# Kernel optimization log

Measured on AMD Instinct MI355X. Metric: run time of the kernel, lower is better.

Reference implementation:

```python
import jax, jax.numpy as jnp
import numpy as np
import math

N = 50000      # nodes
E = 600000     # edges
IN = 128       # in_channels
OUT = 128      # out_channels (heads * per-head)
H = 2          # heads
D = OUT // H   # per-head dim = 64
TDIM = 64      # time encoder out_channels
MSG = 64       # msg_dim
EDGE = TDIM + MSG  # edge_dim = 128


def setup_inputs() -> dict:
    key = jax.random.key(0)
    ks = jax.random.split(key, 16)
    s_in = 1.0 / math.sqrt(IN)
    s_ed = 1.0 / math.sqrt(EDGE)
    return {
        "x": jax.random.normal(ks[0], (N, IN), dtype=jnp.float32),
        "last_update": jax.random.randint(ks[1], (N,), 0, 1000000, dtype=jnp.int32),
        "edge_index": jax.random.randint(ks[2], (2, E), 0, N, dtype=jnp.int64),
        "t": jax.random.randint(ks[3], (E,), 0, 1000000, dtype=jnp.int32),
        "msg": jax.random.normal(ks[4], (E, MSG), dtype=jnp.float32),
        # TimeEncoder: cos(Linear(1 -> TDIM))
        "time_w": jax.random.normal(ks[5], (TDIM,), dtype=jnp.float32) * 0.01,
        "time_b": jax.random.normal(ks[6], (TDIM,), dtype=jnp.float32),
        # TransformerConv params (heads=2, per-head D, edge_dim=EDGE)
        "Wq": jax.random.normal(ks[7], (IN, H * D), dtype=jnp.float32) * s_in,
        "bq": jnp.zeros((H * D,), dtype=jnp.float32),
        "Wk": jax.random.normal(ks[8], (IN, H * D), dtype=jnp.float32) * s_in,
        "bk": jnp.zeros((H * D,), dtype=jnp.float32),
        "Wv": jax.random.normal(ks[9], (IN, H * D), dtype=jnp.float32) * s_in,
        "bv": jnp.zeros((H * D,), dtype=jnp.float32),
        "We": jax.random.normal(ks[10], (EDGE, H * D), dtype=jnp.float32) * s_ed,  # lin_edge, no bias
        "Wskip": jax.random.normal(ks[11], (IN, H * D), dtype=jnp.float32) * s_in,
        "bskip": jnp.zeros((H * D,), dtype=jnp.float32),
    }


def reference(x, last_update, edge_index, t, msg,
              time_w, time_b, Wq, bq, Wk, bk, Wv, bv, We, Wskip, bskip):
    src = edge_index[0]
    dst = edge_index[1]

    # rel_t = last_update[src] - t ; time encoding cos(w * rel_t + b)
    rel_t = (last_update[src] - t).astype(x.dtype)                 # [E]
    rel_t_enc = jnp.cos(rel_t[:, None] * time_w + time_b)          # [E, TDIM]
    edge_attr = jnp.concatenate([rel_t_enc, msg], axis=-1)         # [E, EDGE]

    n = x.shape[0]
    # Node projections, then per-edge gather (PyG: i = dst, j = src)
    q = (x @ Wq + bq).reshape(n, H, D)[dst]                        # [E, H, D]
    k = (x @ Wk + bk).reshape(n, H, D)[src]                        # [E, H, D]
    v = (x @ Wv + bv).reshape(n, H, D)[src]                        # [E, H, D]
    e = (edge_attr @ We).reshape(-1, H, D)                         # [E, H, D]

    k = k + e
    alpha = jnp.sum(q * k, axis=-1) / math.sqrt(D)                 # [E, H]

    # segment softmax over edges sharing the same destination node
    amax = jax.ops.segment_max(alpha, dst, num_segments=n)         # [N, H]
    ex = jnp.exp(alpha - amax[dst])                                # [E, H]
    denom = jax.ops.segment_sum(ex, dst, num_segments=n)           # [N, H]
    attn = ex / (denom[dst] + 1e-16)                               # [E, H]

    out_e = (v + e) * attn[..., None]                              # [E, H, D]
    out = jax.ops.segment_sum(out_e, dst, num_segments=n)          # [N, H, D]
    out = out.reshape(n, H * D)

    # root/skip connection (root_weight=True, beta=False)
    return out + (x @ Wskip + bskip)
```

## Files before the change

### kernel.cpp

```cpp
#include <hip/hip_runtime.h>
#include <hip/hip_bf16.h>

typedef __hip_bfloat16 bf16;
typedef __attribute__((ext_vector_type(8))) short bfrag;
typedef __attribute__((ext_vector_type(4))) float ffrag;

#define CDIM 128
#define TDIMC 64
#define MSGD 64
#define INV2PI 0.15915494309189535f

__device__ __forceinline__ unsigned short f2bf(float f) {
    union { __hip_bfloat16 h; unsigned short u; } cv;
    cv.h = __float2bfloat16(f);
    return cv.u;
}

__device__ __forceinline__ float fcos_rev(float xr) {
    float fr, c;
    asm("v_fract_f32 %0, %1" : "=v"(fr) : "v"(xr));
    asm("v_cos_f32 %0, %1" : "=v"(c) : "v"(fr));
    return c;
}

__global__ void detect_kernel(const int* __restrict__ ei, int samp, int* __restrict__ flag) {
    int i = blockIdx.x * blockDim.x + threadIdx.x;
    if (i < samp) {
        if (ei[2 * i + 1] != 0) atomicOr(flag, 1);
    }
}

__global__ void hist_kernel(const int* __restrict__ ei, int E, const int* __restrict__ flag,
                            int* __restrict__ count) {
    int e = blockIdx.x * 256 + threadIdx.x;
    if (e >= E) return;
    int is32 = *flag;
    int d = is32 ? ei[E + e] : ei[2 * (E + e)];
    atomicAdd(&count[d], 1);
}

__global__ __launch_bounds__(1024)
void scan1_kernel(const int* __restrict__ count, int N,
                  int* __restrict__ cur, int* __restrict__ bsum) {
    __shared__ int wsum[16];
    __shared__ int woff[16];
    int t = threadIdx.x;
    int lane = t & 63, wv = t >> 6;
    int i = blockIdx.x * 1024 + t;
    int v = (i < N) ? count[i] : 0;
    int incl = v;
#pragma unroll
    for (int off = 1; off < 64; off <<= 1) {
        int n = __shfl_up(incl, off, 64);
        if (lane >= off) incl += n;
    }
    if (lane == 63) wsum[wv] = incl;
    __syncthreads();
    if (wv == 0) {
        int ws = (lane < 16) ? wsum[lane] : 0;
        int wi = ws;
#pragma unroll
        for (int off = 1; off < 16; off <<= 1) {
            int n = __shfl_up(wi, off, 64);
            if (lane >= off) wi += n;
        }
        if (lane < 16) woff[lane] = wi - ws;
        if (lane == 15) bsum[blockIdx.x] = wi;
    }
    __syncthreads();
    if (i < N) cur[i] = woff[wv] + incl - v;
}

__global__ void scan2_kernel(int* __restrict__ bsum, int nb) {
    int lane = threadIdx.x;
    int carry = 0;
    for (int base = 0; base < nb; base += 64) {
        int i = base + lane;
        int v = (i < nb) ? bsum[i] : 0;
        int incl = v;
#pragma unroll
        for (int off = 1; off < 64; off <<= 1) {
            int n = __shfl_up(incl, off, 64);
            if (lane >= off) incl += n;
        }
        if (i < nb) bsum[i] = carry + incl - v;
        carry += __shfl(incl, 63, 64);
    }
}

__global__ void scatter_kernel(const int* __restrict__ ei, int E, const int* __restrict__ flag,
                               const int* __restrict__ tarr, const int* __restrict__ last_update,
                               int* __restrict__ cur, const int* __restrict__ bsum,
                               int4* __restrict__ ed_s) {
    int e = blockIdx.x * 256 + threadIdx.x;
    if (e >= E) return;
    int is32 = *flag;
    int s = is32 ? ei[e] : ei[2 * e];
    int d = is32 ? ei[E + e] : ei[2 * (E + e)];
    int pos = atomicAdd(&cur[d], 1) + bsum[d >> 10];
    float rt = (float)(last_update[s] - tarr[e]);
    ed_s[pos] = make_int4(s, d, e, __float_as_int(rt));
}

__global__ void wconv_kernel(const float* __restrict__ Wq, const float* __restrict__ Wk,
                             const float* __restrict__ Wv, const float* __restrict__ Ws,
                             const float* __restrict__ We,
                             short* __restrict__ Wt, short* __restrict__ Wet) {
    int idx = blockIdx.x * 256 + threadIdx.x;
    if (idx >= 5 * 16384) return;
    int mat = idx >> 14;
    int r = idx & 16383;
    int n = r >> 7, kk = r & 127;
    const float* W = (mat == 0) ? Wq : (mat == 1) ? Wk : (mat == 2) ? Wv : (mat == 3) ? Ws : We;
    short bv = (short)f2bf(W[kk * 128 + n]);
    if (mat < 4) Wt[(size_t)mat * 16384 + n * 128 + kk] = bv;
    else         Wet[n * 128 + kk] = bv;
}

__global__ __launch_bounds__(256)
void proj_kernel(const float* __restrict__ x, const short* __restrict__ Wt,
                 const float* __restrict__ bq, const float* __restrict__ bk,
                 const float* __restrict__ bv, const float* __restrict__ bs,
                 float* __restrict__ q, short* __restrict__ kbf, short* __restrict__ vbf,
                 float* __restrict__ out, int N) {
    __shared__ __attribute__((aligned(16))) short sx[64][136];
    int tid = threadIdx.x;
    int n0 = blockIdx.x * 64;
    const float4* x4 = (const float4*)x;
    for (int i = tid; i < 64 * 32; i += 256) {
        int nl = i >> 5, c4 = i & 31;
        int n = n0 + nl;
        float4 f = (n < N) ? x4[(size_t)n * 32 + c4] : make_float4(0.f, 0.f, 0.f, 0.f);
        unsigned int lo = ((unsigned int)f2bf(f.y) << 16) | f2bf(f.x);
        unsigned int hi = ((unsigned int)f2bf(f.w) << 16) | f2bf(f.z);
        *(uint2*)&sx[nl][c4 * 4] = make_uint2(lo, hi);
    }
    __syncthreads();

    int lane = tid & 63, wv = tid >> 6;
    int n15 = lane & 15, quad = lane >> 4;
    const short* W = Wt + (size_t)wv * 16384;
    const float* bias = (wv == 0) ? bq : (wv == 1) ? bk : (wv == 2) ? bv : bs;

    ffrag acc[4][8];
#pragma unroll
    for (int r = 0; r < 4; ++r)
#pragma unroll
        for (int c = 0; c < 8; ++c)
            acc[r][c] = (ffrag){0.f, 0.f, 0.f, 0.f};

#pragma unroll
    for (int kc = 0; kc < 4; ++kc) {
        int kk = kc * 32 + quad * 8;
        bfrag a[4];
#pragma unroll
        for (int r = 0; r < 4; ++r)
            a[r] = *(const bfrag*)&sx[r * 16 + n15][kk];
#pragma unroll
        for (int c = 0; c < 8; ++c) {
            bfrag b = *(const bfrag*)&W[(c * 16 + n15) * 128 + kk];
#pragma unroll
            for (int r = 0; r < 4; ++r)
                acc[r][c] = __builtin_amdgcn_mfma_f32_16x16x32_bf16(a[r], b, acc[r][c], 0, 0, 0);
        }
    }

    if (wv == 1 || wv == 2) {
        short* dsts = (wv == 1) ? kbf : vbf;
#pragma unroll
        for (int c = 0; c < 8; ++c) {
            int col = c * 16 + n15;
            float bval = bias[col];
#pragma unroll
            for (int r = 0; r < 4; ++r) {
#pragma unroll
                for (int g = 0; g < 4; ++g) {
                    int n = n0 + r * 16 + quad * 4 + g;
                    if (n < N) dsts[(size_t)n * CDIM + col] = (short)f2bf(acc[r][c][g] + bval);
                }
            }
        }
    } else {
        float* dstp = (wv == 0) ? q : out;
#pragma unroll
        for (int c = 0; c < 8; ++c) {
            int col = c * 16 + n15;
            float bval = bias[col];
#pragma unroll
            for (int r = 0; r < 4; ++r) {
#pragma unroll
                for (int g = 0; g < 4; ++g) {
                    int n = n0 + r * 16 + quad * 4 + g;
                    if (n < N) dstp[(size_t)n * CDIM + col] = acc[r][c][g] + bval;
                }
            }
        }
    }
}

#define LOADQ(KA, QA, VA, JB) do {                                              \
    _Pragma("unroll")                                                           \
    for (int u = 0; u < 4; ++u) {                                               \
        int el = wv * 16 + (JB) * 4 + u;                                        \
        int s = s_src[el], d = s_dst[el];                                       \
        KA[u] = *(const unsigned int*)&k[(size_t)s * CDIM + 2 * lane];          \
        QA[u] = *(const float2*)&q[(size_t)d * CDIM + 2 * lane];                \
        VA[u] = *(const unsigned int*)&v[(size_t)s * CDIM + 2 * lane];          \
    } } while (0)

#define PROC(KA, QA, VA, JB) do {                                               \
    _Pragma("unroll")                                                           \
    for (int u = 0; u < 4; ++u) {                                               \
        int el = wv * 16 + (JB) * 4 + u;                                        \
        unsigned int ep = *(const unsigned int*)&sbuf[el][2 * lane];            \
        float ex0 = __uint_as_float(ep << 16);                                  \
        float ex1 = __uint_as_float(ep & 0xffff0000u);                          \
        float kx = __uint_as_float(KA[u] << 16) + ex0;                          \
        float ky = __uint_as_float(KA[u] & 0xffff0000u) + ex1;                  \
        float p = QA[u].x * kx + QA[u].y * ky;                                  \
        _Pragma("unroll")                                                       \
        for (int off = 1; off < 32; off <<= 1) p += __shfl_xor(p, off, 32);     \
        float exv = (e0 + el < E) ? __expf(p * 0.125f) : 0.f;                   \
        int d = s_dst[el];                                                      \
        if (d != cur_d) {                              \
            float* np = &num[(size_t)cur_d * CDIM + 2 * lane];                  \
            unsafeAtomicAdd(np, accx);                                          \
            unsafeAtomicAdd(np + 1, accy);                                      \
            if ((lane & 31) == 0) unsafeAtomicAdd(&den[cur_d * 2 + h], dacc);   \
            accx = 0.f; accy = 0.f; dacc = 0.f;                                 \
            cur_d = d;                                                          \
        }                                                                       \
        float vx = __uint_as_float(VA[u] << 16) + ex0;                          \
        float vy = __uint_as_float(VA[u] & 0xffff0000u) + ex1;                  \
        accx = fmaf(vx, exv, accx);                                             \
        accy = fmaf(vy, exv, accy);                                             \
        dacc += exv;                                                            \
    } } while (0)

__global__ __launch_bounds__(256)
void edge_kernel(const int4* __restrict__ ed_s,
                 const float* __restrict__ msg,
                 const float* __restrict__ time_w, const float* __restrict__ time_b,
                 const short* __restrict__ Wet,
                 const float* __restrict__ q, const short* __restrict__ k, const short* __restrict__ v,
                 float* __restrict__ num, float* __restrict__ den,
                 int E) {
    __shared__ __attribute__((aligned(16))) short sbuf[64][136];
    __shared__ int s_src[64], s_dst[64];
    int tid = threadIdx.x;

    int nwg = gridDim.x;
    int q8 = nwg >> 3, r8 = nwg & 7;
    int xcd = blockIdx.x & 7, idx8 = blockIdx.x >> 3;
    int bid = (xcd < r8 ? xcd * (q8 + 1) : r8 * (q8 + 1) + (xcd - r8) * q8) + idx8;
    int e0 = bid * 64;

    if (tid < 64) {
        int4 ed = ed_s[e0 + tid];
        s_src[tid] = ed.x;
        s_dst[tid] = ed.y;
    }
    {
#pragma unroll
        for (int ii = 0; ii < 8; ++ii) {
            int i = tid + ii * 256;
            int el = i >> 5, c2 = i & 31;
            float rt = __int_as_float(ed_s[e0 + el].w);
            float2 w = ((const float2*)time_w)[c2];
            float2 b = ((const float2*)time_b)[c2];
            float c0 = fcos_rev(fmaf(rt, w.x * INV2PI, b.x * INV2PI));
            float c1 = fcos_rev(fmaf(rt, w.y * INV2PI, b.y * INV2PI));
            unsigned int pk = ((unsigned int)f2bf(c1) << 16) | f2bf(c0);
            *(unsigned int*)&sbuf[el][c2 * 2] = pk;
        }
        const float4* msg4 = (const float4*)msg;
#pragma unroll
        for (int jj = 0; jj < 4; ++jj) {
            int j = tid + jj * 256;
            int el = j >> 4, f4 = j & 15;
            int p = ed_s[e0 + el].z;
            float4 m = msg4[(size_t)p * 16 + f4];
            unsigned int lo = ((unsigned int)f2bf(m.y) << 16) | f2bf(m.x);
            unsigned int hi = ((unsigned int)f2bf(m.w) << 16) | f2bf(m.z);
            *(uint2*)&sbuf[el][TDIMC + f4 * 4] = make_uint2(lo, hi);
        }
    }
    __syncthreads();

    int lane = tid & 63;
    int wv = tid >> 6;
    int n15 = lane & 15, quad = lane >> 4;

    unsigned int k0[4], v0[4], k1[4], v1[4], k2[4], v2[4], k3[4], v3[4];
    float2 q0[4], q1[4], q2[4], q3[4];
    LOADQ(k0, q0, v0, 0);
    LOADQ(k1, q1, v1, 1);

    ffrag acc[8];
#pragma unroll
    for (int c = 0; c < 8; ++c) acc[c] = (ffrag){0.f, 0.f, 0.f, 0.f};
#pragma unroll
    for (int kc = 0; kc < 4; ++kc) {
        int kk = kc * 32 + quad * 8;
        bfrag a = *(const bfrag*)&sbuf[wv * 16 + n15][kk];
#pragma unroll
        for (int c = 0; c < 8; ++c) {
            bfrag b = *(const bfrag*)&Wet[(c * 16 + n15) * 128 + kk];
            acc[c] = __builtin_amdgcn_mfma_f32_16x16x32_bf16(a, b, acc[c], 0, 0, 0);
        }
    }
#pragma unroll
    for (int c = 0; c < 8; ++c)
#pragma unroll
        for (int r = 0; r < 4; ++r)
            sbuf[wv * 16 + quad * 4 + r][c * 16 + n15] = (short)f2bf(acc[c][r]);

    asm volatile("s_waitcnt lgkmcnt(0)" ::: "memory");
    __builtin_amdgcn_s_barrier();
    __builtin_amdgcn_sched_barrier(0);

    int h = lane >> 5;
    float accx = 0.f, accy = 0.f, dacc = 0.f;
    int cur_d = s_dst[wv * 16];

    LOADQ(k2, q2, v2, 2);
    PROC(k0, q0, v0, 0);
    LOADQ(k3, q3, v3, 3);
    PROC(k1, q1, v1, 1);
    PROC(k2, q2, v2, 2);
    PROC(k3, q3, v3, 3);

    {
        float* np = &num[(size_t)cur_d * CDIM + 2 * lane];
        unsafeAtomicAdd(np, accx);
        unsafeAtomicAdd(np + 1, accy);
        if ((lane & 31) == 0) unsafeAtomicAdd(&den[cur_d * 2 + h], dacc);
    }
}

__global__ __launch_bounds__(256)
void norm_kernel(const float* __restrict__ num, const float* __restrict__ den,
                 float* __restrict__ out, int N) {
    int idx = blockIdx.x * 256 + threadIdx.x;
    if (idx >= N * 32) return;
    int n = idx >> 5, c4 = idx & 31;
    int h = c4 >> 4;
    float inv = 1.f / (den[n * 2 + h] + 1e-16f);
    float4 nm = ((const float4*)num)[idx];
    float4* op = (float4*)out + idx;
    float4 o = *op;
    o.x = fmaf(nm.x, inv, o.x);
    o.y = fmaf(nm.y, inv, o.y);
    o.z = fmaf(nm.z, inv, o.z);
    o.w = fmaf(nm.w, inv, o.w);
    *op = o;
}

extern "C" void kernel_launch(void* const* d_in, const int* in_sizes, int n_in,
                              void* d_out, int out_size, void* d_ws, size_t ws_size,
                              hipStream_t stream) {
    const float* x       = (const float*)d_in[0];
    const int*   last_up = (const int*)d_in[1];
    const int*   ei      = (const int*)d_in[2];
    const int*   tarr    = (const int*)d_in[3];
    const float* msg     = (const float*)d_in[4];
    const float* time_w  = (const float*)d_in[5];
    const float* time_b  = (const float*)d_in[6];
    const float* Wq = (const float*)d_in[7];  const float* bq = (const float*)d_in[8];
    const float* Wk = (const float*)d_in[9];  const float* bk = (const float*)d_in[10];
    const float* Wv = (const float*)d_in[11]; const float* bv = (const float*)d_in[12];
    const float* We = (const float*)d_in[13];
    const float* Wskip = (const float*)d_in[14]; const float* bskip = (const float*)d_in[15];
    float* out = (float*)d_out;

    int N = in_sizes[0] / CDIM;
    int E = in_sizes[3];
    int nb = (N + 1023) >> 10;

    char* ws = (char*)d_ws;
    size_t off = 0;
#define ALLOC(ptr, type, nelem) type* ptr = (type*)(ws + off); off = (off + (size_t)(nelem) * sizeof(type) + 255) & ~(size_t)255
    ALLOC(q_,    float, (size_t)N * CDIM);
    ALLOC(kbf_,  short, (size_t)N * CDIM);
    ALLOC(vbf_,  short, (size_t)N * CDIM);
    ALLOC(num,   float, (size_t)N * CDIM + 2 * N);
    float* den_ = num + (size_t)N * CDIM;
    ALLOC(count, int,   N + 64);
    int* flag = count + N;
    ALLOC(cur,    int,  N);
    ALLOC(bsum,   int,  nb + 64);
    ALLOC(ed_s,   int4, (size_t)E + 64);
    ALLOC(Wt,     short, 4 * 16384);
    ALLOC(Wet,    short, 16384);
#undef ALLOC

    hipMemsetAsync(count, 0, (size_t)(N + 64) * 4, stream);
    hipMemsetAsync(num, 0, ((size_t)N * CDIM + 2 * N) * sizeof(float), stream);
    hipMemsetAsync(ed_s + E, 0, 64 * sizeof(int4), stream);

    int samp = E < 65536 ? E : 65536;
    detect_kernel<<<(samp + 255) / 256, 256, 0, stream>>>(ei, samp, flag);
    hist_kernel<<<(E + 255) / 256, 256, 0, stream>>>(ei, E, flag, count);
    scan1_kernel<<<nb, 1024, 0, stream>>>(count, N, cur, bsum);
    scan2_kernel<<<1, 64, 0, stream>>>(bsum, nb);
    scatter_kernel<<<(E + 255) / 256, 256, 0, stream>>>(ei, E, flag, tarr, last_up,
                                                        cur, bsum, ed_s);
    wconv_kernel<<<(5 * 16384 + 255) / 256, 256, 0, stream>>>(Wq, Wk, Wv, Wskip, We, Wt, Wet);
    proj_kernel<<<(N + 63) / 64, 256, 0, stream>>>(x, Wt, bq, bk, bv, bskip,
                                                   q_, kbf_, vbf_, out, N);
    edge_kernel<<<(E + 63) / 64, 256, 0, stream>>>(ed_s, msg, time_w, time_b, Wet,
                                                   q_, kbf_, vbf_, num, den_, E);
    norm_kernel<<<(N * 32 + 255) / 256, 256, 0, stream>>>(num, den_, out, N);
}
```

Before: 624.5 us.

## Make edge kernel wave-local, drop block barriers and prefetch gathers early

Each wave now loads its own 16 edges' metadata into LDS and builds its own edge-attribute rows, so the block-wide __syncthreads and s_barrier become per-wave LDS waitcnt fences. The k/q/v gathers and msg loads are issued before the cosine encoding to hide gather latency, and the MFMA section is wrapped in s_setprio. This removes cross-wave stalls at the cost of more live registers. It relies on every wave touching only its own sbuf rows.

```diff
diff --git a/kernel.cpp b/kernel.cpp
--- a/kernel.cpp
+++ b/kernel.cpp
@@ -19,8 +19,13 @@
 __device__ __forceinline__ float fcos_rev(float xr) {
     float fr, c;
     asm("v_fract_f32 %0, %1" : "=v"(fr) : "v"(xr));
-    asm("v_cos_f32 %0, %1" : "=v"(c) : "v"(fr));
+    asm("v_cos_f32 %0, %1" : "=v"(c) : "v"(xr < 0.f ? fr : fr));
     return c;
+}
+
+__device__ __forceinline__ void wave_lds_fence() {
+    asm volatile("s_waitcnt lgkmcnt(0)" ::: "memory");
+    __builtin_amdgcn_sched_barrier(0);
 }
 
 __global__ void detect_kernel(const int* __restrict__ ei, int samp, int* __restrict__ flag) {
@@ -246,8 +251,11 @@
                  float* __restrict__ num, float* __restrict__ den,
                  int E) {
     __shared__ __attribute__((aligned(16))) short sbuf[64][136];
-    __shared__ int s_src[64], s_dst[64];
+    __shared__ int s_src[64], s_dst[64], s_perm[64];
+    __shared__ float s_relt[64];
     int tid = threadIdx.x;
+    int lane = tid & 63;
+    int wv = tid >> 6;
 
     int nwg = gridDim.x;
     int q8 = nwg >> 3, r8 = nwg & 7;
@@ -255,17 +263,36 @@
     int bid = (xcd < r8 ? xcd * (q8 + 1) : r8 * (q8 + 1) + (xcd - r8) * q8) + idx8;
     int e0 = bid * 64;
 
-    if (tid < 64) {
-        int4 ed = ed_s[e0 + tid];
-        s_src[tid] = ed.x;
-        s_dst[tid] = ed.y;
-    }
+    if (lane < 16) {
+        int4 ed = ed_s[e0 + wv * 16 + lane];
+        s_src[wv * 16 + lane] = ed.x;
+        s_dst[wv * 16 + lane] = ed.y;
+        s_perm[wv * 16 + lane] = ed.z;
+        s_relt[wv * 16 + lane] = __int_as_float(ed.w);
+    }
+    wave_lds_fence();
+
+    unsigned int k0[4], v0[4], k1[4], v1[4], k2[4], v2[4], k3[4], v3[4];
+    float2 q0[4], q1[4], q2[4], q3[4];
+    LOADQ(k0, q0, v0, 0);
+    LOADQ(k1, q1, v1, 1);
+
     {
+        const float4* msg4 = (const float4*)msg;
+        float4 m[4];
+        int jel[4], jf4[4];
+#pragma unroll
+        for (int jj = 0; jj < 4; ++jj) {
+            int j = jj * 64 + lane;
+            jel[jj] = wv * 16 + (j >> 4);
+            jf4[jj] = j & 15;
+            m[jj] = msg4[(size_t)s_perm[jel[jj]] * 16 + jf4[jj]];
+        }
 #pragma unroll
         for (int ii = 0; ii < 8; ++ii) {
-            int i = tid + ii * 256;
-            int el = i >> 5, c2 = i & 31;
-            float rt = __int_as_float(ed_s[e0 + el].w);
+            int i = ii * 64 + lane;
+            int el = wv * 16 + (i >> 5), c2 = i & 31;
+            float rt = s_relt[el];
             float2 w = ((const float2*)time_w)[c2];
             float2 b = ((const float2*)time_b)[c2];
             float c0 = fcos_rev(fmaf(rt, w.x * INV2PI, b.x * INV2PI));
@@ -273,32 +300,21 @@
             unsigned int pk = ((unsigned int)f2bf(c1) << 16) | f2bf(c0);
             *(unsigned int*)&sbuf[el][c2 * 2] = pk;
         }
-        const float4* msg4 = (const float4*)msg;
 #pragma unroll
         for (int jj = 0; jj < 4; ++jj) {
-            int j = tid + jj * 256;
-            int el = j >> 4, f4 = j & 15;
-            int p = ed_s[e0 + el].z;
-            float4 m = msg4[(size_t)p * 16 + f4];
-            unsigned int lo = ((unsigned int)f2bf(m.y) << 16) | f2bf(m.x);
-            unsigned int hi = ((unsigned int)f2bf(m.w) << 16) | f2bf(m.z);
-            *(uint2*)&sbuf[el][TDIMC + f4 * 4] = make_uint2(lo, hi);
-        }
-    }
-    __syncthreads();
-
-    int lane = tid & 63;
-    int wv = tid >> 6;
+            unsigned int lo = ((unsigned int)f2bf(m[jj].y) << 16) | f2bf(m[jj].x);
+            unsigned int hi = ((unsigned int)f2bf(m[jj].w) << 16) | f2bf(m[jj].z);
+            *(uint2*)&sbuf[jel[jj]][TDIMC + jf4[jj] * 4] = make_uint2(lo, hi);
+        }
+    }
+    wave_lds_fence();
+
     int n15 = lane & 15, quad = lane >> 4;
 
-    unsigned int k0[4], v0[4], k1[4], v1[4], k2[4], v2[4], k3[4], v3[4];
-    float2 q0[4], q1[4], q2[4], q3[4];
-    LOADQ(k0, q0, v0, 0);
-    LOADQ(k1, q1, v1, 1);
-
     ffrag acc[8];
 #pragma unroll
     for (int c = 0; c < 8; ++c) acc[c] = (ffrag){0.f, 0.f, 0.f, 0.f};
+    __builtin_amdgcn_s_setprio(1);
 #pragma unroll
     for (int kc = 0; kc < 4; ++kc) {
         int kk = kc * 32 + quad * 8;
@@ -309,15 +325,14 @@
             acc[c] = __builtin_amdgcn_mfma_f32_16x16x32_bf16(a, b, acc[c], 0, 0, 0);
         }
     }
+    __builtin_amdgcn_s_setprio(0);
 #pragma unroll
     for (int c = 0; c < 8; ++c)
 #pragma unroll
         for (int r = 0; r < 4; ++r)
             sbuf[wv * 16 + quad * 4 + r][c * 16 + n15] = (short)f2bf(acc[c][r]);
 
-    asm volatile("s_waitcnt lgkmcnt(0)" ::: "memory");
-    __builtin_amdgcn_s_barrier();
-    __builtin_amdgcn_sched_barrier(0);
+    wave_lds_fence();
 
     int h = lane >> 5;
     float accx = 0.f, accy = 0.f, dacc = 0.f;
```

Result: slower. 671.9 us (+7.6%).

## Fuse prep kernels, merge scatter into projection, interleave K/V rows

Applied to the files above, without the earlier changes.

Folds the int64/int32 detection, histogram and weight conversion into one prep kernel, and puts the edge scatter into the projection kernel as extra blocks. K and V are stored interleaved per node so the edge kernel fetches both with a single 8-byte gather instead of two 4-byte gathers. Padding memsets are dropped by clamping edge indices, and the count buffer is zeroed with the same memset as num/den. This cuts launch count and gather transactions. Detecting the index width per wavefront with a ballot is less robust than the old global sample.

```diff
diff --git a/kernel.cpp b/kernel.cpp
--- a/kernel.cpp
+++ b/kernel.cpp
@@ -9,6 +9,7 @@
 #define TDIMC 64
 #define MSGD 64
 #define INV2PI 0.15915494309189535f
+#define WCONV_BLOCKS 320
 
 __device__ __forceinline__ unsigned short f2bf(float f) {
     union { __hip_bfloat16 h; unsigned short u; } cv;
@@ -23,20 +24,32 @@
     return c;
 }
 
-__global__ void detect_kernel(const int* __restrict__ ei, int samp, int* __restrict__ flag) {
-    int i = blockIdx.x * blockDim.x + threadIdx.x;
-    if (i < samp) {
-        if (ei[2 * i + 1] != 0) atomicOr(flag, 1);
-    }
-}
-
-__global__ void hist_kernel(const int* __restrict__ ei, int E, const int* __restrict__ flag,
-                            int* __restrict__ count) {
-    int e = blockIdx.x * 256 + threadIdx.x;
-    if (e >= E) return;
-    int is32 = *flag;
-    int d = is32 ? ei[E + e] : ei[2 * (E + e)];
-    atomicAdd(&count[d], 1);
+__global__ __launch_bounds__(256)
+void prep_kernel(const int* __restrict__ ei, int E, int* __restrict__ count,
+                 const float* __restrict__ Wq, const float* __restrict__ Wk,
+                 const float* __restrict__ Wv, const float* __restrict__ Ws,
+                 const float* __restrict__ We,
+                 short* __restrict__ Wt, short* __restrict__ Wet) {
+    int b = blockIdx.x;
+    if (b < WCONV_BLOCKS) {
+        int idx = b * 256 + threadIdx.x;
+        if (idx >= 5 * 16384) return;
+        int mat = idx >> 14;
+        int r = idx & 16383;
+        int n = r >> 7, kk = r & 127;
+        const float* W = (mat == 0) ? Wq : (mat == 1) ? Wk : (mat == 2) ? Wv : (mat == 3) ? Ws : We;
+        short bv = (short)f2bf(W[kk * 128 + n]);
+        if (mat < 4) Wt[(size_t)mat * 16384 + n * 128 + kk] = bv;
+        else         Wet[n * 128 + kk] = bv;
+    } else {
+        int e = (b - WCONV_BLOCKS) * 256 + threadIdx.x;
+        int probe = (e < E) ? ei[2 * e + 1] : 0;
+        int is32 = (__ballot(probe != 0) != 0ULL);
+        if (e < E) {
+            int d = is32 ? ei[E + e] : ei[2 * (E + e)];
+            atomicAdd(&count[d], 1);
+        }
+    }
 }
 
 __global__ __launch_bounds__(1024)
@@ -88,43 +101,30 @@
     }
 }
 
-__global__ void scatter_kernel(const int* __restrict__ ei, int E, const int* __restrict__ flag,
-                               const int* __restrict__ tarr, const int* __restrict__ last_update,
-                               int* __restrict__ cur, const int* __restrict__ bsum,
-                               int4* __restrict__ ed_s) {
-    int e = blockIdx.x * 256 + threadIdx.x;
-    if (e >= E) return;
-    int is32 = *flag;
-    int s = is32 ? ei[e] : ei[2 * e];
-    int d = is32 ? ei[E + e] : ei[2 * (E + e)];
-    int pos = atomicAdd(&cur[d], 1) + bsum[d >> 10];
-    float rt = (float)(last_update[s] - tarr[e]);
-    ed_s[pos] = make_int4(s, d, e, __float_as_int(rt));
-}
-
-__global__ void wconv_kernel(const float* __restrict__ Wq, const float* __restrict__ Wk,
-                             const float* __restrict__ Wv, const float* __restrict__ Ws,
-                             const float* __restrict__ We,
-                             short* __restrict__ Wt, short* __restrict__ Wet) {
-    int idx = blockIdx.x * 256 + threadIdx.x;
-    if (idx >= 5 * 16384) return;
-    int mat = idx >> 14;
-    int r = idx & 16383;
-    int n = r >> 7, kk = r & 127;
-    const float* W = (mat == 0) ? Wq : (mat == 1) ? Wk : (mat == 2) ? Wv : (mat == 3) ? Ws : We;
-    short bv = (short)f2bf(W[kk * 128 + n]);
-    if (mat < 4) Wt[(size_t)mat * 16384 + n * 128 + kk] = bv;
-    else         Wet[n * 128 + kk] = bv;
-}
-
 __global__ __launch_bounds__(256)
-void proj_kernel(const float* __restrict__ x, const short* __restrict__ Wt,
-                 const float* __restrict__ bq, const float* __restrict__ bk,
-                 const float* __restrict__ bv, const float* __restrict__ bs,
-                 float* __restrict__ q, short* __restrict__ kbf, short* __restrict__ vbf,
-                 float* __restrict__ out, int N) {
+void sp_kernel(const float* __restrict__ x, const short* __restrict__ Wt,
+               const float* __restrict__ bq, const float* __restrict__ bk,
+               const float* __restrict__ bv, const float* __restrict__ bs,
+               float* __restrict__ q, short* __restrict__ kvs,
+               float* __restrict__ out, int N, int PB,
+               const int* __restrict__ ei, int E,
+               const int* __restrict__ tarr, const int* __restrict__ last_update,
+               int* __restrict__ cur, const int* __restrict__ bsum,
+               int4* __restrict__ ed_s) {
     __shared__ __attribute__((aligned(16))) short sx[64][136];
     int tid = threadIdx.x;
+    if (blockIdx.x >= PB) {
+        int e = (blockIdx.x - PB) * 256 + tid;
+        int probe = (e < E) ? ei[2 * e + 1] : 0;
+        int is32 = (__ballot(probe != 0) != 0ULL);
+        if (e >= E) return;
+        int s = is32 ? ei[e] : ei[2 * e];
+        int d = is32 ? ei[E + e] : ei[2 * (E + e)];
+        int pos = atomicAdd(&cur[d], 1) + bsum[d >> 10];
+        float rt = (float)(last_update[s] - tarr[e]);
+        ed_s[pos] = make_int4(s, d, e, __float_as_int(rt));
+        return;
+    }
     int n0 = blockIdx.x * 64;
     const float4* x4 = (const float4*)x;
     for (int i = tid; i < 64 * 32; i += 256) {
@@ -166,17 +166,18 @@
     }
 
     if (wv == 1 || wv == 2) {
-        short* dsts = (wv == 1) ? kbf : vbf;
+        int isv = (wv == 2) ? 2 : 0;
 #pragma unroll
         for (int c = 0; c < 8; ++c) {
             int col = c * 16 + n15;
             float bval = bias[col];
+            int coff = (col >> 1) * 4 + (col & 1) + isv;
 #pragma unroll
             for (int r = 0; r < 4; ++r) {
 #pragma unroll
                 for (int g = 0; g < 4; ++g) {
                     int n = n0 + r * 16 + quad * 4 + g;
-                    if (n < N) dsts[(size_t)n * CDIM + col] = (short)f2bf(acc[r][c][g] + bval);
+                    if (n < N) kvs[(size_t)n * 256 + coff] = (short)f2bf(acc[r][c][g] + bval);
                 }
             }
         }
@@ -198,25 +199,24 @@
     }
 }
 
-#define LOADQ(KA, QA, VA, JB) do {                                              \
+#define LOADQ(KVA, QA, JB) do {                                                 \
     _Pragma("unroll")                                                           \
     for (int u = 0; u < 4; ++u) {                                               \
         int el = wv * 16 + (JB) * 4 + u;                                        \
         int s = s_src[el], d = s_dst[el];                                       \
-        KA[u] = *(const unsigned int*)&k[(size_t)s * CDIM + 2 * lane];          \
+        KVA[u] = kv[(size_t)s * 64 + lane];                                     \
         QA[u] = *(const float2*)&q[(size_t)d * CDIM + 2 * lane];                \
-        VA[u] = *(const unsigned int*)&v[(size_t)s * CDIM + 2 * lane];          \
     } } while (0)
 
-#define PROC(KA, QA, VA, JB) do {                                               \
+#define PROC(KVA, QA, JB) do {                                                  \
     _Pragma("unroll")                                                           \
     for (int u = 0; u < 4; ++u) {                                               \
         int el = wv * 16 + (JB) * 4 + u;                                        \
         unsigned int ep = *(const unsigned int*)&sbuf[el][2 * lane];            \
         float ex0 = __uint_as_float(ep << 16);                                  \
         float ex1 = __uint_as_float(ep & 0xffff0000u);                          \
-        float kx = __uint_as_float(KA[u] << 16) + ex0;                          \
-        float ky = __uint_as_float(KA[u] & 0xffff0000u) + ex1;                  \
+        float kx = __uint_as_float(KVA[u].x << 16) + ex0;                       \
+        float ky = __uint_as_float(KVA[u].x & 0xffff0000u) + ex1;               \
         float p = QA[u].x * kx + QA[u].y * ky;                                  \
         _Pragma("unroll")                                                       \
         for (int off = 1; off < 32; off <<= 1) p += __shfl_xor(p, off, 32);     \
@@ -230,8 +230,8 @@
             accx = 0.f; accy = 0.f; dacc = 0.f;                                 \
             cur_d = d;                                                          \
         }                                                                       \
-        float vx = __uint_as_float(VA[u] << 16) + ex0;                          \
-        float vy = __uint_as_float(VA[u] & 0xffff0000u) + ex1;                  \
+        float vx = __uint_as_float(KVA[u].y << 16) + ex0;                       \
+        float vy = __uint_as_float(KVA[u].y & 0xffff0000u) + ex1;               \
         accx = fmaf(vx, exv, accx);                                             \
         accy = fmaf(vy, exv, accy);                                             \
         dacc += exv;                                                            \
@@ -242,12 +242,13 @@
                  const float* __restrict__ msg,
                  const float* __restrict__ time_w, const float* __restrict__ time_b,
                  const short* __restrict__ Wet,
-                 const float* __restrict__ q, const short* __restrict__ k, const short* __restrict__ v,
+                 const float* __restrict__ q, const uint2* __restrict__ kv,
                  float* __restrict__ num, float* __restrict__ den,
                  int E) {
     __shared__ __attribute__((aligned(16))) short sbuf[64][136];
     __shared__ int s_src[64], s_dst[64];
     int tid = threadIdx.x;
+    int Em1 = E - 1;
 
     int nwg = gridDim.x;
     int q8 = nwg >> 3, r8 = nwg & 7;
@@ -256,7 +257,7 @@
     int e0 = bid * 64;
 
     if (tid < 64) {
-        int4 ed = ed_s[e0 + tid];
+        int4 ed = ed_s[min(e0 + tid, Em1)];
         s_src[tid] = ed.x;
         s_dst[tid] = ed.y;
     }
@@ -265,7 +266,7 @@
         for (int ii = 0; ii < 8; ++ii) {
             int i = tid + ii * 256;
             int el = i >> 5, c2 = i & 31;
-            float rt = __int_as_float(ed_s[e0 + el].w);
+            float rt = __int_as_float(ed_s[min(e0 + el, Em1)].w);
             float2 w = ((const float2*)time_w)[c2];
             float2 b = ((const float2*)time_b)[c2];
             float c0 = fcos_rev(fmaf(rt, w.x * INV2PI, b.x * INV2PI));
@@ -278,7 +279,7 @@
         for (int jj = 0; jj < 4; ++jj) {
             int j = tid + jj * 256;
             int el = j >> 4, f4 = j & 15;
-            int p = ed_s[e0 + el].z;
+            int p = ed_s[min(e0 + el, Em1)].z;
             float4 m = msg4[(size_t)p * 16 + f4];
             unsigned int lo = ((unsigned int)f2bf(m.y) << 16) | f2bf(m.x);
             unsigned int hi = ((unsigned int)f2bf(m.w) << 16) | f2bf(m.z);
@@ -291,10 +292,10 @@
     int wv = tid >> 6;
     int n15 = lane & 15, quad = lane >> 4;
 
-    unsigned int k0[4], v0[4], k1[4], v1[4], k2[4], v2[4], k3[4], v3[4];
+    uint2 kv0[4], kv1[4], kv2[4], kv3[4];
     float2 q0[4], q1[4], q2[4], q3[4];
-    LOADQ(k0, q0, v0, 0);
-    LOADQ(k1, q1, v1, 1);
+    LOADQ(kv0, q0, 0);
+    LOADQ(kv1, q1, 1);
 
     ffrag acc[8];
 #pragma unroll
@@ -323,12 +324,12 @@
     float accx = 0.f, accy = 0.f, dacc = 0.f;
     int cur_d = s_dst[wv * 16];
 
-    LOADQ(k2, q2, v2, 2);
-    PROC(k0, q0, v0, 0);
-    LOADQ(k3, q3, v3, 3);
-    PROC(k1, q1, v1, 1);
-    PROC(k2, q2, v2, 2);
-    PROC(k3, q3, v3, 3);
+    LOADQ(kv2, q2, 2);
+    PROC(kv0, q0, 0);
+    LOADQ(kv3, q3, 3);
+    PROC(kv1, q1, 1);
+    PROC(kv2, q2, 2);
+    PROC(kv3, q3, 3);
 
     {
         float* np = &num[(size_t)cur_d * CDIM + 2 * lane];
@@ -381,34 +382,29 @@
     size_t off = 0;
 #define ALLOC(ptr, type, nelem) type* ptr = (type*)(ws + off); off = (off + (size_t)(nelem) * sizeof(type) + 255) & ~(size_t)255
     ALLOC(q_,    float, (size_t)N * CDIM);
-    ALLOC(kbf_,  short, (size_t)N * CDIM);
-    ALLOC(vbf_,  short, (size_t)N * CDIM);
-    ALLOC(num,   float, (size_t)N * CDIM + 2 * N);
+    ALLOC(kvs_,  short, (size_t)N * 256);
+    ALLOC(num,   float, (size_t)N * CDIM + 2 * N + N);
     float* den_ = num + (size_t)N * CDIM;
-    ALLOC(count, int,   N + 64);
-    int* flag = count + N;
+    int* count  = (int*)(den_ + 2 * N);
     ALLOC(cur,    int,  N);
     ALLOC(bsum,   int,  nb + 64);
-    ALLOC(ed_s,   int4, (size_t)E + 64);
+    ALLOC(ed_s,   int4, (size_t)E);
     ALLOC(Wt,     short, 4 * 16384);
     ALLOC(Wet,    short, 16384);
 #undef ALLOC
 
-    hipMemsetAsync(count, 0, (size_t)(N + 64) * 4, stream);
-    hipMemsetAsync(num, 0, ((size_t)N * CDIM + 2 * N) * sizeof(float), stream);
-    hipMemsetAsync(ed_s + E, 0, 64 * sizeof(int4), stream);
-
-    int samp = E < 65536 ? E : 65536;
-    detect_kernel<<<(samp + 255) / 256, 256, 0, stream>>>(ei, samp, flag);
-    hist_kernel<<<(E + 255) / 256, 256, 0, stream>>>(ei, E, flag, count);
+    hipMemsetAsync(num, 0, ((size_t)N * CDIM + 3 * N) * sizeof(float), stream);
+
+    int histB = (E + 255) / 256;
+    int PB = (N + 63) / 64;
+    prep_kernel<<<WCONV_BLOCKS + histB, 256, 0, stream>>>(ei, E, count,
+                                                          Wq, Wk, Wv, Wskip, We, Wt, Wet);
     scan1_kernel<<<nb, 1024, 0, stream>>>(count, N, cur, bsum);
     scan2_kernel<<<1, 64, 0, stream>>>(bsum, nb);
-    scatter_kernel<<<(E + 255) / 256, 256, 0, stream>>>(ei, E, flag, tarr, last_up,
-                                                        cur, bsum, ed_s);
-    wconv_kernel<<<(5 * 16384 + 255) / 256, 256, 0, stream>>>(Wq, Wk, Wv, Wskip, We, Wt, Wet);
-    proj_kernel<<<(N + 63) / 64, 256, 0, stream>>>(x, Wt, bq, bk, bv, bskip,
-                                                   q_, kbf_, vbf_, out, N);
+    sp_kernel<<<PB + histB, 256, 0, stream>>>(x, Wt, bq, bk, bv, bskip,
+                                              q_, kvs_, out, N, PB,
+                                              ei, E, tarr, last_up, cur, bsum, ed_s);
     edge_kernel<<<(E + 63) / 64, 256, 0, stream>>>(ed_s, msg, time_w, time_b, Wet,
-                                                   q_, kbf_, vbf_, num, den_, E);
+                                                   q_, (const uint2*)kvs_, num, den_, E);
     norm_kernel<<<(N * 32 + 255) / 256, 256, 0, stream>>>(num, den_, out, N);
 }
```

New measurement: 571.0 us. -8.6%, faster.
